# Optimization experiments

Measured on AMD Instinct MI355X. Metric: run time of the kernel, lower is better.

Reference implementation:

```python
import jax, jax.numpy as jnp
import numpy as np
from math import sqrt

B, N, M, HID, NH = 16, 512, 1024, 512, 8
HS = HID // NH  # 64


def layer_norm(x, g, b, eps=1e-5):
    mu = jnp.mean(x, axis=-1, keepdims=True)
    var = jnp.var(x, axis=-1, keepdims=True)
    return (x - mu) * jax.lax.rsqrt(var + eps) * g + b


def apply_moverz(x, s, c):
    # x: [B, L, NH, HS]; s, c: [B, L, 1, HS//2]
    x0, x1 = x[..., 0::2], x[..., 1::2]
    return jnp.concatenate([x0 * c - x1 * s, x1 * c + x0 * s], axis=-1)


def attention(q, k, v, mask):
    # q: [B,Nq,NH,HS], k/v: [B,Nk,NH,HS], mask broadcastable to [B,NH,Nq,Nk]
    attn = jnp.einsum('bnhd,bmhd->bhnm', q, k) / sqrt(HS)
    attn = jnp.where(mask, -jnp.inf, attn)
    attn = jax.nn.softmax(attn, axis=-1)
    x = jnp.einsum('bhnm,bmhd->bnhd', attn, v)
    return x.reshape(x.shape[0], x.shape[1], HID)


def setup_inputs() -> dict:
    key = jax.random.key(0)
    ks = jax.random.split(key, 24)
    inp = {}
    inp['tgt'] = jax.random.normal(ks[0], (B, N, HID), dtype=jnp.float32)
    inp['mem'] = jax.random.normal(ks[1], (B, M, HID), dtype=jnp.float32)
    th_p = jax.random.uniform(ks[2], (B, N, 1, HS // 2), dtype=jnp.float32) * (2 * np.pi)
    th_k = jax.random.uniform(ks[3], (B, M, 1, HS // 2), dtype=jnp.float32) * (2 * np.pi)
    inp['pep_mass_sin'] = jnp.sin(th_p)
    inp['pep_mass_cos'] = jnp.cos(th_p)
    inp['peaks_moverz_sin'] = jnp.sin(th_k)
    inp['peaks_moverz_cos'] = jnp.cos(th_k)
    # causal self-attn mask (True = masked)
    inp['tgt_mask'] = jnp.triu(jnp.ones((N, N), dtype=bool), k=1)[None, None]
    # pad last 64 memory positions
    pad = jnp.arange(M) >= (M - 64)
    inp['mem_key_padding_mask'] = jnp.broadcast_to(pad[None, None, None, :], (B, 1, 1, M))
    s = 0.02
    w = lambda i, shape: jax.random.normal(ks[i], shape, dtype=jnp.float32) * s
    # MaskedMultiHeadAttn params
    inp['mmha_w'] = w(4, (3 * HID, HID)); inp['mmha_b'] = jnp.zeros((3 * HID,), jnp.float32)
    inp['mmha_ow'] = w(5, (HID, HID)); inp['mmha_ob'] = jnp.zeros((HID,), jnp.float32)
    inp['mmha_g'] = jnp.ones((HID,), jnp.float32); inp['mmha_beta'] = jnp.zeros((HID,), jnp.float32)
    # MultiHeadAttn (cross) params
    inp['mha_qw'] = w(6, (HID, HID)); inp['mha_qb'] = jnp.zeros((HID,), jnp.float32)
    inp['mha_kvw'] = w(7, (2 * HID, HID)); inp['mha_kvb'] = jnp.zeros((2 * HID,), jnp.float32)
    inp['mha_ow'] = w(8, (HID, HID)); inp['mha_ob'] = jnp.zeros((HID,), jnp.float32)
    inp['mha_g'] = jnp.ones((HID,), jnp.float32); inp['mha_beta'] = jnp.zeros((HID,), jnp.float32)
    # FFN params (no bias)
    inp['ffn_w1'] = w(9, (4 * HID, HID))
    inp['ffn_w2'] = w(10, (HID, 4 * HID))
    inp['ffn_g'] = jnp.ones((HID,), jnp.float32); inp['ffn_beta'] = jnp.zeros((HID,), jnp.float32)
    return inp


def reference(tgt, mem, pep_mass_sin, pep_mass_cos, peaks_moverz_sin, peaks_moverz_cos,
              tgt_mask, mem_key_padding_mask,
              mmha_w, mmha_b, mmha_ow, mmha_ob, mmha_g, mmha_beta,
              mha_qw, mha_qb, mha_kvw, mha_kvb, mha_ow, mha_ob, mha_g, mha_beta,
              ffn_w1, ffn_w2, ffn_g, ffn_beta):
    # --- masked self-attention ---
    qkv = (tgt @ mmha_w.T + mmha_b).reshape(B, N, NH, 3 * HS)
    q, k, v = jnp.split(qkv, 3, axis=-1)
    x = attention(q, k, v, tgt_mask)
    tgt = layer_norm(x @ mmha_ow.T + mmha_ob + tgt, mmha_g, mmha_beta)
    # --- cross-attention with moverz distance bias ---
    q = (tgt @ mha_qw.T + mha_qb).reshape(B, N, NH, HS)
    q = apply_moverz(q, pep_mass_sin, pep_mass_cos)
    kv = (mem @ mha_kvw.T + mha_kvb).reshape(B, M, NH, 2 * HS)
    k, v = jnp.split(kv, 2, axis=-1)
    k = apply_moverz(k, peaks_moverz_sin, peaks_moverz_cos)
    x = attention(q, k, v, mem_key_padding_mask)
    tgt = layer_norm(x @ mha_ow.T + mha_ob + tgt, mha_g, mha_beta)
    # --- FFN ---
    h = jax.nn.relu(tgt @ ffn_w1.T) @ ffn_w2.T
    tgt = layer_norm(tgt + h, ffn_g, ffn_beta)
    return tgt
```

## Files before the change

### kernel.cpp

```cpp
#include <hip/hip_runtime.h>
#include <hip/hip_bf16.h>

#define BB 16
#define NN 512
#define MM 1024
#define HIDD 512
#define NHH 8

typedef unsigned short ushort_t;
typedef __attribute__((ext_vector_type(8))) short short8;
typedef __attribute__((ext_vector_type(8))) _Float16 half8;
typedef __attribute__((ext_vector_type(4))) _Float16 half4;
typedef __attribute__((ext_vector_type(2))) __fp16 fp16x2;
typedef __attribute__((ext_vector_type(4))) float f32x4;

__device__ __forceinline__ ushort_t f2bf(float x) {
    unsigned u = __float_as_uint(x);
    u += 0x7fff + ((u >> 16) & 1);
    return (ushort_t)(u >> 16);
}

#define GLD16(g, l) __builtin_amdgcn_global_load_lds(                      \
    (const __attribute__((address_space(1))) void*)(g),                    \
    (__attribute__((address_space(3))) void*)(l), 16, 0, 0)

__device__ __forceinline__ void xcd_swizzle(int& colb, int& rowb) {
    int id = blockIdx.x + blockIdx.y * gridDim.x;
    int C = gridDim.x;
    int xcd = id & 7;
    int slot = id >> 3;
    int rows_per = gridDim.y >> 3;
    colb = slot % C;
    rowb = xcd * rows_per + slot / C;
}

__global__ __launch_bounds__(256)
void gemm_bf(const ushort_t* __restrict__ A, const ushort_t* __restrict__ W,
             const float* __restrict__ bias, float* __restrict__ C,
             ushort_t* __restrict__ Cb, _Float16* __restrict__ Ch,
             int K, int Cout, int relu) {
    __shared__ __align__(16) ushort_t smem[2][8192];
    const int tid = threadIdx.x;
    const int lane = tid & 63;
    const int wid = tid >> 6;
    const int wm = wid >> 1, wn = wid & 1;
    int colb, rowb;
    xcd_swizzle(colb, rowb);
    const long row0 = (long)rowb * 128;
    const long col0 = (long)colb * 128;

    const int sr = lane >> 2;
    const int skq = lane & 3;
    const ushort_t* Ag = A + (row0 + wid * 32 + sr) * (long)K + skq * 8;
    const ushort_t* Wg = W + (col0 + wid * 32 + sr) * (long)K + skq * 8;
    const int sa0 = (wid * 32) * 32, sa1 = (wid * 32 + 16) * 32;

    f32x4 acc[4][4] = {};
    const int lr = lane & 15;
    const int kg = lane >> 4;

    GLD16(Ag, &smem[0][sa0]);
    GLD16(Ag + 16 * (long)K, &smem[0][sa1]);
    GLD16(Wg, &smem[0][4096 + sa0]);
    GLD16(Wg + 16 * (long)K, &smem[0][4096 + sa1]);

    int pb = 0;
    for (int k0 = 0; k0 < K; k0 += 32, pb ^= 1) {
        __syncthreads();
        int kn = k0 + 32;
        if (kn < K) {
            GLD16(Ag + kn, &smem[pb ^ 1][sa0]);
            GLD16(Ag + 16 * (long)K + kn, &smem[pb ^ 1][sa1]);
            GLD16(Wg + kn, &smem[pb ^ 1][4096 + sa0]);
            GLD16(Wg + 16 * (long)K + kn, &smem[pb ^ 1][4096 + sa1]);
        }
        const ushort_t* Ab = smem[pb];
        const ushort_t* Wb = smem[pb] + 4096;
        short8 af[4], bfr[4];
#pragma unroll
        for (int i = 0; i < 4; i++)
            af[i] = *(const short8*)&Ab[(wm * 64 + i * 16 + lr) * 32 + kg * 8];
#pragma unroll
        for (int j = 0; j < 4; j++)
            bfr[j] = *(const short8*)&Wb[(wn * 64 + j * 16 + lr) * 32 + kg * 8];
#pragma unroll
        for (int i = 0; i < 4; i++)
#pragma unroll
            for (int j = 0; j < 4; j++)
                acc[i][j] = __builtin_amdgcn_mfma_f32_16x16x32_bf16(
                    af[i], bfr[j], acc[i][j], 0, 0, 0);
    }

#pragma unroll
    for (int i = 0; i < 4; i++) {
#pragma unroll
        for (int j = 0; j < 4; j++) {
            long row = row0 + wm * 64 + i * 16 + kg * 4;
            long col = col0 + wn * 64 + j * 16 + lr;
            float bv = bias ? bias[col] : 0.f;
#pragma unroll
            for (int r = 0; r < 4; r++) {
                float x = acc[i][j][r] + bv;
                if (relu) x = fmaxf(x, 0.f);
                size_t idx = (row + r) * (size_t)Cout + col;
                if (Ch)      Ch[idx] = (_Float16)x;
                else if (Cb) Cb[idx] = f2bf(x);
                else         C[idx] = x;
            }
        }
    }
}

__global__ __launch_bounds__(256)
void gemm_bf64(const ushort_t* __restrict__ A, const ushort_t* __restrict__ W,
               const float* __restrict__ bias, float* __restrict__ C,
               ushort_t* __restrict__ Cb, _Float16* __restrict__ Ch,
               int K, int Cout, int relu) {
    __shared__ __align__(16) ushort_t smem[2][6144];
    const int tid = threadIdx.x;
    const int lane = tid & 63;
    const int w = tid >> 6;
    int colb, rowb;
    xcd_swizzle(colb, rowb);
    const long row0 = (long)rowb * 128;
    const long col0 = (long)colb * 64;

    const int sr = lane >> 2;
    const int skq = lane & 3;
    const ushort_t* Ag = A + (row0 + w * 32 + sr) * (long)K + skq * 8;
    const ushort_t* Wg = W + (col0 + w * 16 + sr) * (long)K + skq * 8;
    const int sa0 = (w * 32) * 32, sa1 = (w * 32 + 16) * 32;
    const int sw0 = 4096 + (w * 16) * 32;

    f32x4 acc[2][4] = {};
    const int lr = lane & 15;
    const int kg = lane >> 4;

    GLD16(Ag, &smem[0][sa0]);
    GLD16(Ag + 16 * (long)K, &smem[0][sa1]);
    GLD16(Wg, &smem[0][sw0]);

    int pb = 0;
    for (int k0 = 0; k0 < K; k0 += 32, pb ^= 1) {
        __syncthreads();
        int kn = k0 + 32;
        if (kn < K) {
            GLD16(Ag + kn, &smem[pb ^ 1][sa0]);
            GLD16(Ag + 16 * (long)K + kn, &smem[pb ^ 1][sa1]);
            GLD16(Wg + kn, &smem[pb ^ 1][sw0]);
        }
        const ushort_t* Ab = smem[pb];
        const ushort_t* Wb = smem[pb] + 4096;
        short8 af[2], bfr[4];
#pragma unroll
        for (int i = 0; i < 2; i++)
            af[i] = *(const short8*)&Ab[(w * 32 + i * 16 + lr) * 32 + kg * 8];
#pragma unroll
        for (int j = 0; j < 4; j++)
            bfr[j] = *(const short8*)&Wb[(j * 16 + lr) * 32 + kg * 8];
#pragma unroll
        for (int i = 0; i < 2; i++)
#pragma unroll
            for (int j = 0; j < 4; j++)
                acc[i][j] = __builtin_amdgcn_mfma_f32_16x16x32_bf16(
                    af[i], bfr[j], acc[i][j], 0, 0, 0);
    }

#pragma unroll
    for (int i = 0; i < 2; i++) {
#pragma unroll
        for (int j = 0; j < 4; j++) {
            long row = row0 + w * 32 + i * 16 + kg * 4;
            long col = col0 + j * 16 + lr;
            float bv = bias ? bias[col] : 0.f;
#pragma unroll
            for (int r = 0; r < 4; r++) {
                float x = acc[i][j][r] + bv;
                if (relu) x = fmaxf(x, 0.f);
                size_t idx = (row + r) * (size_t)Cout + col;
                if (Ch)      Ch[idx] = (_Float16)x;
                else if (Cb) Cb[idx] = f2bf(x);
                else         C[idx] = x;
            }
        }
    }
}

__global__ __launch_bounds__(256)
void gemm_bf64_sk(const ushort_t* __restrict__ A, const ushort_t* __restrict__ W,
                  int lda, int Kslice, float* __restrict__ C0,
                  float* __restrict__ C1, int Cout) {
    __shared__ __align__(16) ushort_t smem[2][6144];
    const int tid = threadIdx.x;
    const int lane = tid & 63;
    const int w = tid >> 6;
    int colb, rowb;
    xcd_swizzle(colb, rowb);
    const long row0 = (long)rowb * 128;
    const long col0 = (long)colb * 64;
    const long koff = (long)blockIdx.z * Kslice;
    float* __restrict__ C = blockIdx.z ? C1 : C0;

    const int sr = lane >> 2;
    const int skq = lane & 3;
    const ushort_t* Ag = A + (row0 + w * 32 + sr) * (long)lda + koff + skq * 8;
    const ushort_t* Wg = W + (col0 + w * 16 + sr) * (long)lda + koff + skq * 8;
    const int sa0 = (w * 32) * 32, sa1 = (w * 32 + 16) * 32;
    const int sw0 = 4096 + (w * 16) * 32;

    f32x4 acc[2][4] = {};
    const int lr = lane & 15;
    const int kg = lane >> 4;

    GLD16(Ag, &smem[0][sa0]);
    GLD16(Ag + 16 * (long)lda, &smem[0][sa1]);
    GLD16(Wg, &smem[0][sw0]);

    int pb = 0;
    for (int k0 = 0; k0 < Kslice; k0 += 32, pb ^= 1) {
        __syncthreads();
        int kn = k0 + 32;
        if (kn < Kslice) {
            GLD16(Ag + kn, &smem[pb ^ 1][sa0]);
            GLD16(Ag + 16 * (long)lda + kn, &smem[pb ^ 1][sa1]);
            GLD16(Wg + kn, &smem[pb ^ 1][sw0]);
        }
        const ushort_t* Ab = smem[pb];
        const ushort_t* Wb = smem[pb] + 4096;
        short8 af[2], bfr[4];
#pragma unroll
        for (int i = 0; i < 2; i++)
            af[i] = *(const short8*)&Ab[(w * 32 + i * 16 + lr) * 32 + kg * 8];
#pragma unroll
        for (int j = 0; j < 4; j++)
            bfr[j] = *(const short8*)&Wb[(j * 16 + lr) * 32 + kg * 8];
#pragma unroll
        for (int i = 0; i < 2; i++)
#pragma unroll
            for (int j = 0; j < 4; j++)
                acc[i][j] = __builtin_amdgcn_mfma_f32_16x16x32_bf16(
                    af[i], bfr[j], acc[i][j], 0, 0, 0);
    }

#pragma unroll
    for (int i = 0; i < 2; i++)
#pragma unroll
        for (int j = 0; j < 4; j++) {
            long row = row0 + w * 32 + i * 16 + kg * 4;
            long col = col0 + j * 16 + lr;
#pragma unroll
            for (int r = 0; r < 4; r++)
                C[(row + r) * (size_t)Cout + col] = acc[i][j][r];
        }
}

__global__ __launch_bounds__(256)
void gemm_q_rot(const ushort_t* __restrict__ A, const ushort_t* __restrict__ W,
                const float* __restrict__ bias,
                const float* __restrict__ sn, const float* __restrict__ cs,
                _Float16* __restrict__ Qrot) {
    __shared__ __align__(16) ushort_t smem[2][6144];
    _Float16* Cs = (_Float16*)smem;
    const int K = 512;
    const int tid = threadIdx.x;
    const int lane = tid & 63;
    const int w = tid >> 6;
    int colb, rowb;
    xcd_swizzle(colb, rowb);
    const long row0 = (long)rowb * 128;
    const int h = colb;
    const long col0 = (long)h * 64;

    const int sr = lane >> 2;
    const int skq = lane & 3;
    const ushort_t* Ag = A + (row0 + w * 32 + sr) * (long)K + skq * 8;
    const ushort_t* Wg = W + (col0 + w * 16 + sr) * (long)K + skq * 8;
    const int sa0 = (w * 32) * 32, sa1 = (w * 32 + 16) * 32;
    const int sw0 = 4096 + (w * 16) * 32;

    f32x4 acc[2][4] = {};
    const int lr = lane & 15;
    const int kg = lane >> 4;

    GLD16(Ag, &smem[0][sa0]);
    GLD16(Ag + 16 * (long)K, &smem[0][sa1]);
    GLD16(Wg, &smem[0][sw0]);

    int pb = 0;
    for (int k0 = 0; k0 < K; k0 += 32, pb ^= 1) {
        __syncthreads();
        int kn = k0 + 32;
        if (kn < K) {
            GLD16(Ag + kn, &smem[pb ^ 1][sa0]);
            GLD16(Ag + 16 * (long)K + kn, &smem[pb ^ 1][sa1]);
            GLD16(Wg + kn, &smem[pb ^ 1][sw0]);
        }
        const ushort_t* Ab = smem[pb];
        const ushort_t* Wb = smem[pb] + 4096;
        short8 af[2], bfr[4];
#pragma unroll
        for (int i = 0; i < 2; i++)
            af[i] = *(const short8*)&Ab[(w * 32 + i * 16 + lr) * 32 + kg * 8];
#pragma unroll
        for (int j = 0; j < 4; j++)
            bfr[j] = *(const short8*)&Wb[(j * 16 + lr) * 32 + kg * 8];
#pragma unroll
        for (int i = 0; i < 2; i++)
#pragma unroll
            for (int j = 0; j < 4; j++)
                acc[i][j] = __builtin_amdgcn_mfma_f32_16x16x32_bf16(
                    af[i], bfr[j], acc[i][j], 0, 0, 0);
    }

    __syncthreads();
#pragma unroll
    for (int i = 0; i < 2; i++)
#pragma unroll
        for (int j = 0; j < 4; j++) {
            int row = w * 32 + i * 16 + kg * 4;
            int col = j * 16 + lr;
            float bv = bias[col0 + col];
#pragma unroll
            for (int r = 0; r < 4; r++)
                Cs[(row + r) * 76 + col] = (_Float16)(acc[i][j][r] + bv);
        }
    __syncthreads();
    for (int idx = tid; idx < 4096; idx += 256) {
        int rr = idx >> 5, j = idx & 31;
        size_t srow = (size_t)row0 + rr;
        float x0 = (float)Cs[rr * 76 + 2 * j], x1 = (float)Cs[rr * 76 + 2 * j + 1];
        float s = sn[srow * 32 + j], c = cs[srow * 32 + j];
        Qrot[srow * 512 + h * 64 + j]      = (_Float16)(x0 * c - x1 * s);
        Qrot[srow * 512 + h * 64 + 32 + j] = (_Float16)(x1 * c + x0 * s);
    }
}

__global__ __launch_bounds__(256)
void gemm_kv(const ushort_t* __restrict__ A, const ushort_t* __restrict__ W,
             const float* __restrict__ bias,
             const float* __restrict__ sn, const float* __restrict__ cs,
             _Float16* __restrict__ Krot, _Float16* __restrict__ Vth) {
    __shared__ __align__(16) ushort_t smem[2][8192];
    _Float16* Cs = (_Float16*)smem;
    const int K = 512;
    const int tid = threadIdx.x;
    const int lane = tid & 63;
    const int wid = tid >> 6;
    const int wm = wid >> 1, wn = wid & 1;
    int colb, rowb;
    xcd_swizzle(colb, rowb);
    const long row0 = (long)rowb * 128;
    const int h = colb;
    const long col0 = (long)h * 128;

    const int sr = lane >> 2;
    const int skq = lane & 3;
    const ushort_t* Ag = A + (row0 + wid * 32 + sr) * (long)K + skq * 8;
    const ushort_t* Wg = W + (col0 + wid * 32 + sr) * (long)K + skq * 8;
    const int sa0 = (wid * 32) * 32, sa1 = (wid * 32 + 16) * 32;

    f32x4 acc[4][4] = {};
    const int lr = lane & 15;
    const int kg = lane >> 4;

    GLD16(Ag, &smem[0][sa0]);
    GLD16(Ag + 16 * (long)K, &smem[0][sa1]);
    GLD16(Wg, &smem[0][4096 + sa0]);
    GLD16(Wg + 16 * (long)K, &smem[0][4096 + sa1]);

    int pb = 0;
    for (int k0 = 0; k0 < K; k0 += 32, pb ^= 1) {
        __syncthreads();
        int kn = k0 + 32;
        if (kn < K) {
            GLD16(Ag + kn, &smem[pb ^ 1][sa0]);
            GLD16(Ag + 16 * (long)K + kn, &smem[pb ^ 1][sa1]);
            GLD16(Wg + kn, &smem[pb ^ 1][4096 + sa0]);
            GLD16(Wg + 16 * (long)K + kn, &smem[pb ^ 1][4096 + sa1]);
        }
        const ushort_t* Ab = smem[pb];
        const ushort_t* Wb = smem[pb] + 4096;
        short8 af[4], bfr[4];
#pragma unroll
        for (int i = 0; i < 4; i++)
            af[i] = *(const short8*)&Ab[(wm * 64 + i * 16 + lr) * 32 + kg * 8];
#pragma unroll
        for (int j = 0; j < 4; j++)
            bfr[j] = *(const short8*)&Wb[(wn * 64 + j * 16 + lr) * 32 + kg * 8];
#pragma unroll
        for (int i = 0; i < 4; i++)
#pragma unroll
            for (int j = 0; j < 4; j++)
                acc[i][j] = __builtin_amdgcn_mfma_f32_16x16x32_bf16(
                    af[i], bfr[j], acc[i][j], 0, 0, 0);
    }

    const int b_ = (int)(row0 >> 10);
    const int m0_ = (int)(row0 & 1023);
#pragma unroll
    for (int half = 0; half < 2; half++) {
        __syncthreads();
        if (wn == half) {
#pragma unroll
            for (int i = 0; i < 4; i++)
#pragma unroll
                for (int j = 0; j < 4; j++) {
                    int row = wm * 64 + i * 16 + kg * 4;
                    int col = j * 16 + lr;
                    float bv = bias[col0 + half * 64 + col];
#pragma unroll
                    for (int r = 0; r < 4; r++)
                        Cs[(row + r) * 76 + col] = (_Float16)(acc[i][j][r] + bv);
                }
        }
        __syncthreads();
        if (half == 0) {
            for (int idx = tid; idx < 4096; idx += 256) {
                int rr = idx >> 5, j = idx & 31;
                size_t srow = (size_t)row0 + rr;
                float x0 = (float)Cs[rr * 76 + 2 * j], x1 = (float)Cs[rr * 76 + 2 * j + 1];
                float s = sn[srow * 32 + j], c = cs[srow * 32 + j];
                Krot[srow * 512 + h * 64 + j]      = (_Float16)(x0 * c - x1 * s);
                Krot[srow * 512 + h * 64 + 32 + j] = (_Float16)(x1 * c + x0 * s);
            }
        } else {
            for (int idx = tid; idx < 1024; idx += 256) {
                int d = idx >> 4, c = idx & 15;
                half8 v;
#pragma unroll
                for (int k = 0; k < 8; k++) v[k] = Cs[(c * 8 + k) * 76 + d];
                *(half8*)(Vth + (((size_t)(b_ * NHH + h)) * 64 + d) * MM
                          + m0_ + c * 8) = v;
            }
        }
    }
}

__global__ __launch_bounds__(256)
void cvt_all(const float* __restrict__ tgt, const float* __restrict__ mem,
             const float* __restrict__ w0, const float* __restrict__ w1,
             const float* __restrict__ w2, const float* __restrict__ w3,
             const float* __restrict__ w4, const float* __restrict__ w5,
             const float* __restrict__ w6,
             ushort_t* __restrict__ Abf, ushort_t* __restrict__ membf,
             ushort_t* __restrict__ Wbf) {
    int blk = blockIdx.x;
    const float* src;
    ushort_t* dst;
    size_t off;
    if (blk < 4096)       { src = tgt; dst = Abf;   off = (size_t)blk * 1024; }
    else if (blk < 12288) { src = mem; dst = membf; off = (size_t)(blk - 4096) * 1024; }
    else {
        int wb = blk - 12288;
        dst = Wbf + (size_t)wb * 1024;
        if (wb < 768)       { src = w0; off = (size_t)wb * 1024; }
        else if (wb < 1024) { src = w1; off = (size_t)(wb - 768) * 1024; }
        else if (wb < 1280) { src = w2; off = (size_t)(wb - 1024) * 1024; }
        else if (wb < 1792) { src = w3; off = (size_t)(wb - 1280) * 1024; }
        else if (wb < 2048) { src = w4; off = (size_t)(wb - 1792) * 1024; }
        else if (wb < 3072) { src = w5; off = (size_t)(wb - 2048) * 1024; }
        else                { src = w6; off = (size_t)(wb - 3072) * 1024; }
        float4 v = *(const float4*)(src + off + threadIdx.x * 4);
        ushort4 o;
        o.x = f2bf(v.x); o.y = f2bf(v.y); o.z = f2bf(v.z); o.w = f2bf(v.w);
        *(ushort4*)(dst + threadIdx.x * 4) = o;
        return;
    }
    float4 v = *(const float4*)(src + off + threadIdx.x * 4);
    ushort4 o;
    o.x = f2bf(v.x); o.y = f2bf(v.y); o.z = f2bf(v.z); o.w = f2bf(v.w);
    *(ushort4*)(dst + off + threadIdx.x * 4) = o;
}

__global__ __launch_bounds__(256)
void prep_vt(const _Float16* __restrict__ src, int L, int stride,
             int hmul, int hadd, _Float16* __restrict__ Vt) {
    const int b = blockIdx.z, h = blockIdx.y, m0 = blockIdx.x * 64;
    const int tid = threadIdx.x;
    __shared__ _Float16 vt[64][72];
    for (int idx = tid; idx < 512; idx += 256) {
        int m = idx >> 3, c = idx & 7;
        half8 v = *(const half8*)(src + ((size_t)(b * L + m0 + m)) * stride
                                  + h * hmul + hadd + c * 8);
#pragma unroll
        for (int k = 0; k < 8; k++) vt[c * 8 + k][m] = v[k];
    }
    __syncthreads();
    for (int idx = tid; idx < 512; idx += 256) {
        int d = idx >> 3, c = idx & 7;
        *(half8*)(Vt + (((size_t)(b * NHH + h)) * 64 + d) * L + m0 + c * 8)
            = *(const half8*)&vt[d][c * 8];
    }
}

__global__ __launch_bounds__(512, 4)
void attn10(const _Float16* __restrict__ Q, int qstride, int qmul, int qadd,
            const _Float16* __restrict__ K, int kstride, int kmul, int kadd,
            const _Float16* __restrict__ Vt, int LV, int Lrows,
            ushort_t* __restrict__ out, int kvlen, int causal) {
    const int g = blockIdx.x;
    const int bh = (g & 7) * 16 + ((g >> 3) & 15);
    int qb = g >> 7;
    qb ^= (qb & 2) >> 1;
    const int b = bh >> 3, h = bh & 7;
    const int n0 = qb * 128;
    const int tid = threadIdx.x, lane = tid & 63, w = tid >> 6;
    const int quad = lane >> 4, l16 = lane & 15;
    const int qw = n0 + w * 16;

    __shared__ _Float16 Ks[2][64 * 64];
    __shared__ _Float16 Vs[2][64 * 64];
    __shared__ _Float16 Ps[8][16 * 64];
    _Float16* Pw = Ps[w];

    half8 bq[2];
#pragma unroll
    for (int c = 0; c < 2; c++)
        bq[c] = *(const half8*)(Q + ((size_t)(b * NN + qw + l16)) * qstride
                                + h * qmul + qadd + c * 32 + quad * 8);

    f32x4 acc[4] = {};
    float mrun = -3e38f, lrun = 0.f;

    const int srow = tid >> 3;
    const int scol = tid & 7;
    const int ssw = (scol ^ (srow & 7)) * 8;

    const int limit = causal ? (n0 + 128) : kvlen;
    const int nt = limit >> 6;

    const size_t kbase = ((size_t)(b * Lrows)) * kstride + h * kmul + kadd;
    const size_t vbase = (((size_t)(b * NHH + h)) * 64 + srow) * (size_t)LV;

    half8 kr = *(const half8*)(K + kbase + (size_t)srow * kstride + scol * 8);
    half8 vr = *(const half8*)(Vt + vbase + scol * 8);
    *(half8*)&Ks[0][srow * 64 + ssw] = kr;
    *(half8*)&Vs[0][srow * 64 + ssw] = vr;
    if (nt > 1) {
        kr = *(const half8*)(K + kbase + (size_t)(64 + srow) * kstride + scol * 8);
        vr = *(const half8*)(Vt + vbase + 64 + scol * 8);
    }

    const float SC = 0.125f * 1.44269504f;
    const int fsw = l16 & 7;
    int pb = 0;
    for (int t = 0; t < nt; t++, pb ^= 1) {
        const int key0 = t * 64;
        __syncthreads();
        if (t + 1 < nt) {
            *(half8*)&Ks[pb ^ 1][srow * 64 + ssw] = kr;
            *(half8*)&Vs[pb ^ 1][srow * 64 + ssw] = vr;
            if (t + 2 < nt) {
                kr = *(const half8*)(K + kbase
                        + (size_t)((t + 2) * 64 + srow) * kstride + scol * 8);
                vr = *(const half8*)(Vt + vbase + (t + 2) * 64 + scol * 8);
            }
        }
        if (causal && key0 > qw + 15) continue;

        const _Float16* Kb = Ks[pb];
        const _Float16* Vb = Vs[pb];
        f32x4 st[4];
        __builtin_amdgcn_s_setprio(1);
#pragma unroll
        for (int kt = 0; kt < 4; kt++) {
            const int rk = kt * 16 + l16;
            half8 ak0 = *(const half8*)&Kb[rk * 64 + ((quad ^ fsw) * 8)];
            half8 ak1 = *(const half8*)&Kb[rk * 64 + (((quad + 4) ^ fsw) * 8)];
            f32x4 z = {};
            z = __builtin_amdgcn_mfma_f32_16x16x32_f16(ak0, bq[0], z, 0, 0, 0);
            z = __builtin_amdgcn_mfma_f32_16x16x32_f16(ak1, bq[1], z, 0, 0, 0);
            st[kt] = z;
        }
        __builtin_amdgcn_s_setprio(0);

        if (causal && key0 + 64 > qw) {
            const int qabs = qw + l16;
#pragma unroll
            for (int kt = 0; kt < 4; kt++)
#pragma unroll
                for (int r = 0; r < 4; r++)
                    if (key0 + kt * 16 + quad * 4 + r > qabs)
                        st[kt][r] = -3e38f;
        }

        float plm = -3e38f;
#pragma unroll
        for (int kt = 0; kt < 4; kt++)
            plm = fmaxf(plm, fmaxf(fmaxf(st[kt][0], st[kt][1]),
                                   fmaxf(st[kt][2], st[kt][3])));

        const int keep = __all(plm - mrun <= 64.f);
        if (!keep) {
            float lm = fmaxf(plm, __shfl_xor(plm, 16));
            lm = fmaxf(lm, __shfl_xor(lm, 32));
            float mnew = fmaxf(mrun, lm);
            float corr = exp2f((mrun - mnew) * SC);
            mrun = mnew;
            lrun *= corr;
            float cb0 = __shfl(corr, (lane & 48) | (quad * 4 + 0));
            float cb1 = __shfl(corr, (lane & 48) | (quad * 4 + 1));
            float cb2 = __shfl(corr, (lane & 48) | (quad * 4 + 2));
            float cb3 = __shfl(corr, (lane & 48) | (quad * 4 + 3));
#pragma unroll
            for (int dt = 0; dt < 4; dt++) {
                acc[dt][0] *= cb0; acc[dt][1] *= cb1;
                acc[dt][2] *= cb2; acc[dt][3] *= cb3;
            }
        }
        const float mb = mrun * SC;
#pragma unroll
        for (int kt = 0; kt < 4; kt++) {
            float p0 = exp2f(__builtin_fmaf(st[kt][0], SC, -mb));
            float p1 = exp2f(__builtin_fmaf(st[kt][1], SC, -mb));
            float p2 = exp2f(__builtin_fmaf(st[kt][2], SC, -mb));
            float p3 = exp2f(__builtin_fmaf(st[kt][3], SC, -mb));
            lrun += (p0 + p1) + (p2 + p3);
            fp16x2 lo = __builtin_amdgcn_cvt_pkrtz(p0, p1);
            fp16x2 hi = __builtin_amdgcn_cvt_pkrtz(p2, p3);
            union { unsigned u[2]; half4 h; } pk;
            pk.u[0] = __builtin_bit_cast(unsigned, lo);
            pk.u[1] = __builtin_bit_cast(unsigned, hi);
            int jc = 2 * kt + (quad >> 1);
            *(half4*)&Pw[l16 * 64 + ((jc ^ fsw) * 8) + (quad & 1) * 4] = pk.h;
        }
        half8 ap[2];
#pragma unroll
        for (int c = 0; c < 2; c++)
            ap[c] = *(const half8*)&Pw[l16 * 64 + (((c * 4 + quad) ^ fsw) * 8)];
        __builtin_amdgcn_s_setprio(1);
#pragma unroll
        for (int dt = 0; dt < 4; dt++) {
            const int rv = dt * 16 + l16;
            half8 bv0 = *(const half8*)&Vb[rv * 64 + ((quad ^ fsw) * 8)];
            half8 bv1 = *(const half8*)&Vb[rv * 64 + (((quad + 4) ^ fsw) * 8)];
            acc[dt] = __builtin_amdgcn_mfma_f32_16x16x32_f16(ap[0], bv0, acc[dt], 0, 0, 0);
            acc[dt] = __builtin_amdgcn_mfma_f32_16x16x32_f16(ap[1], bv1, acc[dt], 0, 0, 0);
        }
        __builtin_amdgcn_s_setprio(0);
    }

    lrun += __shfl_xor(lrun, 16);
    lrun += __shfl_xor(lrun, 32);
    float invq = 1.f / lrun;
    float iv0 = __shfl(invq, (lane & 48) | (quad * 4 + 0));
    float iv1 = __shfl(invq, (lane & 48) | (quad * 4 + 1));
    float iv2 = __shfl(invq, (lane & 48) | (quad * 4 + 2));
    float iv3 = __shfl(invq, (lane & 48) | (quad * 4 + 3));
#pragma unroll
    for (int dt = 0; dt < 4; dt++) {
        size_t base = ((size_t)(b * NN + qw + quad * 4)) * 512
                      + h * 64 + dt * 16 + l16;
        out[base]           = f2bf(acc[dt][0] * iv0);
        out[base + 512]     = f2bf(acc[dt][1] * iv1);
        out[base + 1024]    = f2bf(acc[dt][2] * iv2);
        out[base + 1536]    = f2bf(acc[dt][3] * iv3);
    }
}

__global__ __launch_bounds__(256)
void ln_residual(const float* __restrict__ u, const float* __restrict__ u2,
                 const float* __restrict__ res,
                 const float* __restrict__ g, const float* __restrict__ be,
                 float* __restrict__ out, ushort_t* __restrict__ outbf) {
    const int row = blockIdx.x, t = threadIdx.x;
    const float* rp = res + (size_t)row * HIDD;
    const float* up = u + (size_t)row * HIDD;
    float z0 = rp[t] + up[t];
    float z1 = rp[t + 256] + up[t + 256];
    if (u2) {
        const float* up2 = u2 + (size_t)row * HIDD;
        z0 += up2[t];
        z1 += up2[t + 256];
    }
    float sm = z0 + z1, s2 = z0 * z0 + z1 * z1;
#pragma unroll
    for (int off = 1; off < 64; off <<= 1) {
        sm += __shfl_xor(sm, off, 64);
        s2 += __shfl_xor(s2, off, 64);
    }
    __shared__ float ps[4], ps2[4];
    int w = t >> 6;
    if ((t & 63) == 0) { ps[w] = sm; ps2[w] = s2; }
    __syncthreads();
    sm = ps[0] + ps[1] + ps[2] + ps[3];
    s2 = ps2[0] + ps2[1] + ps2[2] + ps2[3];
    float mu = sm * (1.f / 512.f);
    float var = s2 * (1.f / 512.f) - mu * mu;
    float rstd = rsqrtf(var + 1e-5f);
    float y0 = (z0 - mu) * rstd * g[t] + be[t];
    float y1 = (z1 - mu) * rstd * g[t + 256] + be[t + 256];
    out[(size_t)row * HIDD + t]       = y0;
    out[(size_t)row * HIDD + t + 256] = y1;
    if (outbf) {
        outbf[(size_t)row * HIDD + t]       = f2bf(y0);
        outbf[(size_t)row * HIDD + t + 256] = f2bf(y1);
    }
}

extern "C" void kernel_launch(void* const* d_in, const int* in_sizes, int n_in,
                              void* d_out, int out_size, void* d_ws, size_t ws_size,
                              hipStream_t stream) {
    const float* tgt      = (const float*)d_in[0];
    const float* mem      = (const float*)d_in[1];
    const float* pep_sin  = (const float*)d_in[2];
    const float* pep_cos  = (const float*)d_in[3];
    const float* pk_sin   = (const float*)d_in[4];
    const float* pk_cos   = (const float*)d_in[5];
    const float* mmha_w   = (const float*)d_in[8];
    const float* mmha_b   = (const float*)d_in[9];
    const float* mmha_ow  = (const float*)d_in[10];
    const float* mmha_ob  = (const float*)d_in[11];
    const float* mmha_g   = (const float*)d_in[12];
    const float* mmha_be  = (const float*)d_in[13];
    const float* mha_qw   = (const float*)d_in[14];
    const float* mha_qb   = (const float*)d_in[15];
    const float* mha_kvw  = (const float*)d_in[16];
    const float* mha_kvb  = (const float*)d_in[17];
    const float* mha_ow   = (const float*)d_in[18];
    const float* mha_ob   = (const float*)d_in[19];
    const float* mha_g    = (const float*)d_in[20];
    const float* mha_be   = (const float*)d_in[21];
    const float* ffn_w1   = (const float*)d_in[22];
    const float* ffn_w2   = (const float*)d_in[23];
    const float* ffn_g    = (const float*)d_in[24];
    const float* ffn_be   = (const float*)d_in[25];

    float* ws = (float*)d_ws;
    float* utmp  = ws;
    float* tgt12 = ws + 4194304;
    _Float16* hp = (_Float16*)(ws + 8388608);
    _Float16* qkvh  = hp;
    _Float16* Qrot  = hp + 12582912;
    _Float16* Vth   = hp + 16777216;
    _Float16* Krot  = hp + 25165824;
    ushort_t* membf = (ushort_t*)(hp + 33554432);
    ushort_t* Abf   = (ushort_t*)(hp + 41943040);
    ushort_t* Wbf   = (ushort_t*)(hp + 46137344);
    ushort_t* w_mmha = Wbf;
    ushort_t* w_mmow = Wbf + 786432;
    ushort_t* w_qw   = Wbf + 1048576;
    ushort_t* w_kvw  = Wbf + 1310720;
    ushort_t* w_mow  = Wbf + 1835008;
    ushort_t* w_f1   = Wbf + 2097152;
    ushort_t* w_f2   = Wbf + 3145728;
    ushort_t* hbf = (ushort_t*)qkvh;
    float* utmp2 = (float*)Krot;
    float* out = (float*)d_out;
    (void)in_sizes; (void)n_in; (void)out_size; (void)ws_size;

    cvt_all<<<16384, 256, 0, stream>>>(tgt, mem, mmha_w, mmha_ow, mha_qw,
                                       mha_kvw, mha_ow, ffn_w1, ffn_w2,
                                       Abf, membf, Wbf);
    gemm_bf<<<dim3(12, 64), 256, 0, stream>>>(Abf, w_mmha, mmha_b, nullptr, nullptr, qkvh, 512, 1536, 0);
    prep_vt<<<dim3(8, NHH, BB), 256, 0, stream>>>(qkvh, NN, 1536, 192, 128, Vth);
    attn10<<<512, 512, 0, stream>>>(qkvh, 1536, 192, 0, qkvh, 1536, 192, 64,
                                    Vth, NN, NN, Abf, 0, 1);
    gemm_bf64<<<dim3(8, 64), 256, 0, stream>>>(Abf, w_mmow, mmha_ob, utmp, nullptr, nullptr, 512, 512, 0);
    ln_residual<<<8192, 256, 0, stream>>>(utmp, nullptr, tgt, mmha_g, mmha_be, tgt12, Abf);
    gemm_q_rot<<<dim3(8, 64), 256, 0, stream>>>(Abf, w_qw, mha_qb, pep_sin, pep_cos, Qrot);
    gemm_kv<<<dim3(8, 128), 256, 0, stream>>>(membf, w_kvw, mha_kvb, pk_sin, pk_cos, Krot, Vth);
    attn10<<<512, 512, 0, stream>>>(Qrot, 512, 64, 0, Krot, 512, 64, 0,
                                    Vth, MM, MM, Abf, MM - 64, 0);
    gemm_bf64<<<dim3(8, 64), 256, 0, stream>>>(Abf, w_mow, mha_ob, utmp, nullptr, nullptr, 512, 512, 0);
    ln_residual<<<8192, 256, 0, stream>>>(utmp, nullptr, tgt12, mha_g, mha_be, tgt12, Abf);
    gemm_bf<<<dim3(16, 64), 256, 0, stream>>>(Abf, w_f1, nullptr, nullptr, hbf, nullptr, 512, 2048, 1);
    gemm_bf64_sk<<<dim3(8, 64, 2), 256, 0, stream>>>(hbf, w_f2, 2048, 1024, utmp, utmp2, 512);
    ln_residual<<<8192, 256, 0, stream>>>(utmp, utmp2, tgt12, ffn_g, ffn_be, out, nullptr);
}
```

Before: 397.6 us.

## Merge self-QKV and cross-KV GEMMs into one launch; shrink attention blocks

Merges the self-attention QKV projection and the memory KV projection (with rotary and V transpose) into a single launch of 1792 blocks. The goal is to fill the GPU better and remove one launch. Self-attention V now gets its own workspace buffer so the two outputs do not collide. The attention kernel moves to 64-query blocks of 256 threads, giving 1024 blocks, with a permuted block order for the causal case. It drops the per-warp skip of fully masked causal tiles, which may add some wasted work on the diagonal tiles.

After: 395.0 us. Within noise of the previous version (-0.7%).

```diff
diff --git a/kernel.cpp b/kernel.cpp
--- a/kernel.cpp
+++ b/kernel.cpp
@@ -32,6 +32,14 @@
     int rows_per = gridDim.y >> 3;
     colb = slot % C;
     rowb = xcd * rows_per + slot / C;
+}
+
+__device__ __forceinline__ void xcd_swz_p(int id, int C, int Rdiv8,
+                                          int& colb, int& rowb) {
+    int xcd = id & 7;
+    int slot = id >> 3;
+    colb = slot % C;
+    rowb = xcd * Rdiv8 + slot / C;
 }
 
 __global__ __launch_bounds__(256)
@@ -106,6 +114,166 @@
                 if (Ch)      Ch[idx] = (_Float16)x;
                 else if (Cb) Cb[idx] = f2bf(x);
                 else         C[idx] = x;
+            }
+        }
+    }
+}
+
+__global__ __launch_bounds__(256)
+void gemm_qkv_kv(const ushort_t* __restrict__ A, const ushort_t* __restrict__ Wq,
+                 const float* __restrict__ bq, _Float16* __restrict__ qkvh,
+                 const ushort_t* __restrict__ Mem, const ushort_t* __restrict__ Wkv,
+                 const float* __restrict__ bkv,
+                 const float* __restrict__ sn, const float* __restrict__ cs,
+                 _Float16* __restrict__ Krot, _Float16* __restrict__ Vth) {
+    __shared__ __align__(16) ushort_t smem[2][8192];
+    const int tid = threadIdx.x;
+    const int lane = tid & 63;
+    const int wid = tid >> 6;
+    const int lr = lane & 15;
+    const int kg = lane >> 4;
+    const int sr = lane >> 2;
+    const int skq = lane & 3;
+    const int K = 512;
+
+    if (blockIdx.x < 768) {
+        int colb, rowb;
+        xcd_swz_p(blockIdx.x, 12, 8, colb, rowb);
+        const long row0 = (long)rowb * 128;
+        const long col0 = (long)colb * 128;
+        const int wm = wid >> 1, wn = wid & 1;
+        const ushort_t* Ag = A + (row0 + wid * 32 + sr) * (long)K + skq * 8;
+        const ushort_t* Wg = Wq + (col0 + wid * 32 + sr) * (long)K + skq * 8;
+        const int sa0 = (wid * 32) * 32, sa1 = (wid * 32 + 16) * 32;
+
+        f32x4 acc[4][4] = {};
+        GLD16(Ag, &smem[0][sa0]);
+        GLD16(Ag + 16 * (long)K, &smem[0][sa1]);
+        GLD16(Wg, &smem[0][4096 + sa0]);
+        GLD16(Wg + 16 * (long)K, &smem[0][4096 + sa1]);
+
+        int pb = 0;
+        for (int k0 = 0; k0 < K; k0 += 32, pb ^= 1) {
+            __syncthreads();
+            int kn = k0 + 32;
+            if (kn < K) {
+                GLD16(Ag + kn, &smem[pb ^ 1][sa0]);
+                GLD16(Ag + 16 * (long)K + kn, &smem[pb ^ 1][sa1]);
+                GLD16(Wg + kn, &smem[pb ^ 1][4096 + sa0]);
+                GLD16(Wg + 16 * (long)K + kn, &smem[pb ^ 1][4096 + sa1]);
+            }
+            const ushort_t* Ab = smem[pb];
+            const ushort_t* Wb = smem[pb] + 4096;
+            short8 af[4], bfr[4];
+#pragma unroll
+            for (int i = 0; i < 4; i++)
+                af[i] = *(const short8*)&Ab[(wm * 64 + i * 16 + lr) * 32 + kg * 8];
+#pragma unroll
+            for (int j = 0; j < 4; j++)
+                bfr[j] = *(const short8*)&Wb[(wn * 64 + j * 16 + lr) * 32 + kg * 8];
+#pragma unroll
+            for (int i = 0; i < 4; i++)
+#pragma unroll
+                for (int j = 0; j < 4; j++)
+                    acc[i][j] = __builtin_amdgcn_mfma_f32_16x16x32_bf16(
+                        af[i], bfr[j], acc[i][j], 0, 0, 0);
+        }
+
+#pragma unroll
+        for (int i = 0; i < 4; i++)
+#pragma unroll
+            for (int j = 0; j < 4; j++) {
+                long row = row0 + wm * 64 + i * 16 + kg * 4;
+                long col = col0 + wn * 64 + j * 16 + lr;
+                float bv = bq[col];
+#pragma unroll
+                for (int r = 0; r < 4; r++)
+                    qkvh[(row + r) * (size_t)1536 + col] =
+                        (_Float16)(acc[i][j][r] + bv);
+            }
+    } else {
+        _Float16* Cs = (_Float16*)smem;
+        int colb, rowb;
+        xcd_swz_p(blockIdx.x - 768, 8, 16, colb, rowb);
+        const long row0 = (long)rowb * 128;
+        const int h = colb;
+        const long col0 = (long)h * 128;
+        const int wm = wid >> 1, wn = wid & 1;
+        const ushort_t* Ag = Mem + (row0 + wid * 32 + sr) * (long)K + skq * 8;
+        const ushort_t* Wg = Wkv + (col0 + wid * 32 + sr) * (long)K + skq * 8;
+        const int sa0 = (wid * 32) * 32, sa1 = (wid * 32 + 16) * 32;
+
+        f32x4 acc[4][4] = {};
+        GLD16(Ag, &smem[0][sa0]);
+        GLD16(Ag + 16 * (long)K, &smem[0][sa1]);
+        GLD16(Wg, &smem[0][4096 + sa0]);
+        GLD16(Wg + 16 * (long)K, &smem[0][4096 + sa1]);
+
+        int pb = 0;
+        for (int k0 = 0; k0 < K; k0 += 32, pb ^= 1) {
+            __syncthreads();
+            int kn = k0 + 32;
+            if (kn < K) {
+                GLD16(Ag + kn, &smem[pb ^ 1][sa0]);
+                GLD16(Ag + 16 * (long)K + kn, &smem[pb ^ 1][sa1]);
+                GLD16(Wg + kn, &smem[pb ^ 1][4096 + sa0]);
+                GLD16(Wg + 16 * (long)K + kn, &smem[pb ^ 1][4096 + sa1]);
+            }
+            const ushort_t* Ab = smem[pb];
+            const ushort_t* Wb = smem[pb] + 4096;
+            short8 af[4], bfr[4];
+#pragma unroll
+            for (int i = 0; i < 4; i++)
+                af[i] = *(const short8*)&Ab[(wm * 64 + i * 16 + lr) * 32 + kg * 8];
+#pragma unroll
+            for (int j = 0; j < 4; j++)
+                bfr[j] = *(const short8*)&Wb[(wn * 64 + j * 16 + lr) * 32 + kg * 8];
+#pragma unroll
+            for (int i = 0; i < 4; i++)
+#pragma unroll
+                for (int j = 0; j < 4; j++)
+                    acc[i][j] = __builtin_amdgcn_mfma_f32_16x16x32_bf16(
+                        af[i], bfr[j], acc[i][j], 0, 0, 0);
+        }
+
+        const int b_ = (int)(row0 >> 10);
+        const int m0_ = (int)(row0 & 1023);
+#pragma unroll
+        for (int half = 0; half < 2; half++) {
+            __syncthreads();
+            if (wn == half) {
+#pragma unroll
+                for (int i = 0; i < 4; i++)
+#pragma unroll
+                    for (int j = 0; j < 4; j++) {
+                        int row = wm * 64 + i * 16 + kg * 4;
+                        int col = j * 16 + lr;
+                        float bv = bkv[col0 + half * 64 + col];
+#pragma unroll
+                        for (int r = 0; r < 4; r++)
+                            Cs[(row + r) * 76 + col] = (_Float16)(acc[i][j][r] + bv);
+                    }
+            }
+            __syncthreads();
+            if (half == 0) {
+                for (int idx = tid; idx < 4096; idx += 256) {
+                    int rr = idx >> 5, j = idx & 31;
+                    size_t srow = (size_t)row0 + rr;
+                    float x0 = (float)Cs[rr * 76 + 2 * j];
+                    float x1 = (float)Cs[rr * 76 + 2 * j + 1];
+                    float s = sn[srow * 32 + j], c = cs[srow * 32 + j];
+                    Krot[srow * 512 + h * 64 + j]      = (_Float16)(x0 * c - x1 * s);
+                    Krot[srow * 512 + h * 64 + 32 + j] = (_Float16)(x1 * c + x0 * s);
+                }
+            } else {
+                for (int idx = tid; idx < 1024; idx += 256) {
+                    int d = idx >> 4, c = idx & 15;
+                    half8 v;
+#pragma unroll
+                    for (int k = 0; k < 8; k++) v[k] = Cs[(c * 8 + k) * 76 + d];
+                    *(half8*)(Vth + (((size_t)(b_ * NHH + h)) * 64 + d) * MM
+                              + m0_ + c * 8) = v;
+                }
             }
         }
     }
@@ -332,107 +500,6 @@
         float s = sn[srow * 32 + j], c = cs[srow * 32 + j];
         Qrot[srow * 512 + h * 64 + j]      = (_Float16)(x0 * c - x1 * s);
         Qrot[srow * 512 + h * 64 + 32 + j] = (_Float16)(x1 * c + x0 * s);
-    }
-}
-
-__global__ __launch_bounds__(256)
-void gemm_kv(const ushort_t* __restrict__ A, const ushort_t* __restrict__ W,
-             const float* __restrict__ bias,
-             const float* __restrict__ sn, const float* __restrict__ cs,
-             _Float16* __restrict__ Krot, _Float16* __restrict__ Vth) {
-    __shared__ __align__(16) ushort_t smem[2][8192];
-    _Float16* Cs = (_Float16*)smem;
-    const int K = 512;
-    const int tid = threadIdx.x;
-    const int lane = tid & 63;
-    const int wid = tid >> 6;
-    const int wm = wid >> 1, wn = wid & 1;
-    int colb, rowb;
-    xcd_swizzle(colb, rowb);
-    const long row0 = (long)rowb * 128;
-    const int h = colb;
-    const long col0 = (long)h * 128;
-
-    const int sr = lane >> 2;
-    const int skq = lane & 3;
-    const ushort_t* Ag = A + (row0 + wid * 32 + sr) * (long)K + skq * 8;
-    const ushort_t* Wg = W + (col0 + wid * 32 + sr) * (long)K + skq * 8;
-    const int sa0 = (wid * 32) * 32, sa1 = (wid * 32 + 16) * 32;
-
-    f32x4 acc[4][4] = {};
-    const int lr = lane & 15;
-    const int kg = lane >> 4;
-
-    GLD16(Ag, &smem[0][sa0]);
-    GLD16(Ag + 16 * (long)K, &smem[0][sa1]);
-    GLD16(Wg, &smem[0][4096 + sa0]);
-    GLD16(Wg + 16 * (long)K, &smem[0][4096 + sa1]);
-
-    int pb = 0;
-    for (int k0 = 0; k0 < K; k0 += 32, pb ^= 1) {
-        __syncthreads();
-        int kn = k0 + 32;
-        if (kn < K) {
-            GLD16(Ag + kn, &smem[pb ^ 1][sa0]);
-            GLD16(Ag + 16 * (long)K + kn, &smem[pb ^ 1][sa1]);
-            GLD16(Wg + kn, &smem[pb ^ 1][4096 + sa0]);
-            GLD16(Wg + 16 * (long)K + kn, &smem[pb ^ 1][4096 + sa1]);
-        }
-        const ushort_t* Ab = smem[pb];
-        const ushort_t* Wb = smem[pb] + 4096;
-        short8 af[4], bfr[4];
-#pragma unroll
-        for (int i = 0; i < 4; i++)
-            af[i] = *(const short8*)&Ab[(wm * 64 + i * 16 + lr) * 32 + kg * 8];
-#pragma unroll
-        for (int j = 0; j < 4; j++)
-            bfr[j] = *(const short8*)&Wb[(wn * 64 + j * 16 + lr) * 32 + kg * 8];
-#pragma unroll
-        for (int i = 0; i < 4; i++)
-#pragma unroll
-            for (int j = 0; j < 4; j++)
-                acc[i][j] = __builtin_amdgcn_mfma_f32_16x16x32_bf16(
-                    af[i], bfr[j], acc[i][j], 0, 0, 0);
-    }
-
-    const int b_ = (int)(row0 >> 10);
-    const int m0_ = (int)(row0 & 1023);
-#pragma unroll
-    for (int half = 0; half < 2; half++) {
-        __syncthreads();
-        if (wn == half) {
-#pragma unroll
-            for (int i = 0; i < 4; i++)
-#pragma unroll
-                for (int j = 0; j < 4; j++) {
-                    int row = wm * 64 + i * 16 + kg * 4;
-                    int col = j * 16 + lr;
-                    float bv = bias[col0 + half * 64 + col];
-#pragma unroll
-                    for (int r = 0; r < 4; r++)
-                        Cs[(row + r) * 76 + col] = (_Float16)(acc[i][j][r] + bv);
-                }
-        }
-        __syncthreads();
-        if (half == 0) {
-            for (int idx = tid; idx < 4096; idx += 256) {
-                int rr = idx >> 5, j = idx & 31;
-                size_t srow = (size_t)row0 + rr;
-                float x0 = (float)Cs[rr * 76 + 2 * j], x1 = (float)Cs[rr * 76 + 2 * j + 1];
-                float s = sn[srow * 32 + j], c = cs[srow * 32 + j];
-                Krot[srow * 512 + h * 64 + j]      = (_Float16)(x0 * c - x1 * s);
-                Krot[srow * 512 + h * 64 + 32 + j] = (_Float16)(x1 * c + x0 * s);
-            }
-        } else {
-            for (int idx = tid; idx < 1024; idx += 256) {
-                int d = idx >> 4, c = idx & 15;
-                half8 v;
-#pragma unroll
-                for (int k = 0; k < 8; k++) v[k] = Cs[(c * 8 + k) * 76 + d];
-                *(half8*)(Vth + (((size_t)(b_ * NHH + h)) * 64 + d) * MM
-                          + m0_ + c * 8) = v;
-            }
-        }
     }
 }
 
@@ -493,24 +560,24 @@
     }
 }
 
-__global__ __launch_bounds__(512, 4)
-void attn10(const _Float16* __restrict__ Q, int qstride, int qmul, int qadd,
+__global__ __launch_bounds__(256, 4)
+void attn11(const _Float16* __restrict__ Q, int qstride, int qmul, int qadd,
             const _Float16* __restrict__ K, int kstride, int kmul, int kadd,
             const _Float16* __restrict__ Vt, int LV, int Lrows,
             ushort_t* __restrict__ out, int kvlen, int causal) {
     const int g = blockIdx.x;
     const int bh = (g & 7) * 16 + ((g >> 3) & 15);
-    int qb = g >> 7;
-    qb ^= (qb & 2) >> 1;
+    const int qraw = g >> 7;
+    const int qb = causal ? ((0x12476530u >> (qraw << 2)) & 7) : qraw;
     const int b = bh >> 3, h = bh & 7;
-    const int n0 = qb * 128;
+    const int n0 = qb * 64;
     const int tid = threadIdx.x, lane = tid & 63, w = tid >> 6;
     const int quad = lane >> 4, l16 = lane & 15;
     const int qw = n0 + w * 16;
 
     __shared__ _Float16 Ks[2][64 * 64];
     __shared__ _Float16 Vs[2][64 * 64];
-    __shared__ _Float16 Ps[8][16 * 64];
+    __shared__ _Float16 Ps[4][16 * 64];
     _Float16* Pw = Ps[w];
 
     half8 bq[2];
@@ -526,19 +593,30 @@
     const int scol = tid & 7;
     const int ssw = (scol ^ (srow & 7)) * 8;
 
-    const int limit = causal ? (n0 + 128) : kvlen;
+    const int limit = causal ? (n0 + 64) : kvlen;
     const int nt = limit >> 6;
 
     const size_t kbase = ((size_t)(b * Lrows)) * kstride + h * kmul + kadd;
     const size_t vbase = (((size_t)(b * NHH + h)) * 64 + srow) * (size_t)LV;
 
-    half8 kr = *(const half8*)(K + kbase + (size_t)srow * kstride + scol * 8);
-    half8 vr = *(const half8*)(Vt + vbase + scol * 8);
-    *(half8*)&Ks[0][srow * 64 + ssw] = kr;
-    *(half8*)&Vs[0][srow * 64 + ssw] = vr;
+    half8 kr0, kr1, vr0, vr1;
+    {
+        size_t kb = kbase + (size_t)srow * kstride + scol * 8;
+        kr0 = *(const half8*)(K + kb);
+        kr1 = *(const half8*)(K + kb + (size_t)32 * kstride);
+        vr0 = *(const half8*)(Vt + vbase + scol * 8);
+        vr1 = *(const half8*)(Vt + vbase + (size_t)32 * LV + scol * 8);
+    }
+    *(half8*)&Ks[0][srow * 64 + ssw] = kr0;
+    *(half8*)&Ks[0][(srow + 32) * 64 + ssw] = kr1;
+    *(half8*)&Vs[0][srow * 64 + ssw] = vr0;
+    *(half8*)&Vs[0][(srow + 32) * 64 + ssw] = vr1;
     if (nt > 1) {
-        kr = *(const half8*)(K + kbase + (size_t)(64 + srow) * kstride + scol * 8);
-        vr = *(const half8*)(Vt + vbase + 64 + scol * 8);
+        size_t kb = kbase + (size_t)(64 + srow) * kstride + scol * 8;
+        kr0 = *(const half8*)(K + kb);
+        kr1 = *(const half8*)(K + kb + (size_t)32 * kstride);
+        vr0 = *(const half8*)(Vt + vbase + 64 + scol * 8);
+        vr1 = *(const half8*)(Vt + vbase + (size_t)32 * LV + 64 + scol * 8);
     }
 
     const float SC = 0.125f * 1.44269504f;
@@ -548,15 +626,19 @@
         const int key0 = t * 64;
         __syncthreads();
         if (t + 1 < nt) {
-            *(half8*)&Ks[pb ^ 1][srow * 64 + ssw] = kr;
-            *(half8*)&Vs[pb ^ 1][srow * 64 + ssw] = vr;
+            *(half8*)&Ks[pb ^ 1][srow * 64 + ssw] = kr0;
+            *(half8*)&Ks[pb ^ 1][(srow + 32) * 64 + ssw] = kr1;
+            *(half8*)&Vs[pb ^ 1][srow * 64 + ssw] = vr0;
+            *(half8*)&Vs[pb ^ 1][(srow + 32) * 64 + ssw] = vr1;
             if (t + 2 < nt) {
-                kr = *(const half8*)(K + kbase
-                        + (size_t)((t + 2) * 64 + srow) * kstride + scol * 8);
-                vr = *(const half8*)(Vt + vbase + (t + 2) * 64 + scol * 8);
+                size_t kb = kbase + (size_t)((t + 2) * 64 + srow) * kstride + scol * 8;
+                kr0 = *(const half8*)(K + kb);
+                kr1 = *(const half8*)(K + kb + (size_t)32 * kstride);
+                vr0 = *(const half8*)(Vt + vbase + (t + 2) * 64 + scol * 8);
+                vr1 = *(const half8*)(Vt + vbase + (size_t)32 * LV
+                                      + (t + 2) * 64 + scol * 8);
             }
         }
-        if (causal && key0 > qw + 15) continue;
 
         const _Float16* Kb = Ks[pb];
         const _Float16* Vb = Vs[pb];
@@ -744,6 +826,7 @@
     ushort_t* w_mow  = Wbf + 1835008;
     ushort_t* w_f1   = Wbf + 2097152;
     ushort_t* w_f2   = Wbf + 3145728;
+    _Float16* Vth_self = hp + 50331648;
     ushort_t* hbf = (ushort_t*)qkvh;
     float* utmp2 = (float*)Krot;
     float* out = (float*)d_out;
@@ -752,16 +835,17 @@
     cvt_all<<<16384, 256, 0, stream>>>(tgt, mem, mmha_w, mmha_ow, mha_qw,
                                        mha_kvw, mha_ow, ffn_w1, ffn_w2,
                                        Abf, membf, Wbf);
-    gemm_bf<<<dim3(12, 64), 256, 0, stream>>>(Abf, w_mmha, mmha_b, nullptr, nullptr, qkvh, 512, 1536, 0);
-    prep_vt<<<dim3(8, NHH, BB), 256, 0, stream>>>(qkvh, NN, 1536, 192, 128, Vth);
-    attn10<<<512, 512, 0, stream>>>(qkvh, 1536, 192, 0, qkvh, 1536, 192, 64,
-                                    Vth, NN, NN, Abf, 0, 1);
+    gemm_qkv_kv<<<1792, 256, 0, stream>>>(Abf, w_mmha, mmha_b, qkvh,
+                                          membf, w_kvw, mha_kvb,
+                                          pk_sin, pk_cos, Krot, Vth);
+    prep_vt<<<dim3(8, NHH, BB), 256, 0, stream>>>(qkvh, NN, 1536, 192, 128, Vth_self);
+    attn11<<<1024, 256, 0, stream>>>(qkvh, 1536, 192, 0, qkvh, 1536, 192, 64,
+                                     Vth_self, NN, NN, Abf, 0, 1);
     gemm_bf64<<<dim3(8, 64), 256, 0, stream>>>(Abf, w_mmow, mmha_ob, utmp, nullptr, nullptr, 512, 512, 0);
     ln_residual<<<8192, 256, 0, stream>>>(utmp, nullptr, tgt, mmha_g, mmha_be, tgt12, Abf);
     gemm_q_rot<<<dim3(8, 64), 256, 0, stream>>>(Abf, w_qw, mha_qb, pep_sin, pep_cos, Qrot);
-    gemm_kv<<<dim3(8, 128), 256, 0, stream>>>(membf, w_kvw, mha_kvb, pk_sin, pk_cos, Krot, Vth);
-    attn10<<<512, 512, 0, stream>>>(Qrot, 512, 64, 0, Krot, 512, 64, 0,
-                                    Vth, MM, MM, Abf, MM - 64, 0);
+    attn11<<<1024, 256, 0, stream>>>(Qrot, 512, 64, 0, Krot, 512, 64, 0,
+                                     Vth, MM, MM, Abf, MM - 64, 0);
     gemm_bf64<<<dim3(8, 64), 256, 0, stream>>>(Abf, w_mow, mha_ob, utmp, nullptr, nullptr, 512, 512, 0);
     ln_residual<<<8192, 256, 0, stream>>>(utmp, nullptr, tgt12, mha_g, mha_be, tgt12, Abf);
     gemm_bf<<<dim3(16, 64), 256, 0, stream>>>(Abf, w_f1, nullptr, nullptr, hbf, nullptr, 512, 2048, 1);
```
